# Kernel tuning notes

Measured on AMD Instinct MI355X. Metric: run time of the kernel, lower is better.

The kernel has to match this reference:

```python
import jax, jax.numpy as jnp
import numpy as np

EPS = 1e-8
PHI = (1 + 5 ** 0.5) / 2
B, S, D, H, L, O = 8, 2048, 256, 512, 3, 1
NH = 4
HD = H // NH


def setup_inputs() -> dict:
    key = jax.random.key(0)
    ks = jax.random.split(key, 12)
    g = lambda k, shape, s=0.02: jax.random.normal(k, shape, dtype=jnp.float32) * s
    # Fibonacci modular spiral embedding (fixed, requires_grad=False in torch)
    idx = jnp.arange(D, dtype=jnp.float32)
    r = (PHI * idx) % 1.0
    th = 2 * jnp.pi * r
    phase_emb = jnp.stack([r * jnp.cos(th), r * jnp.sin(th)], axis=1)  # [D,2]
    return dict(
        x=jax.random.normal(ks[0], (B, S, D), dtype=jnp.float32),
        proj_w=g(ks[1], (D, D), 0.06), proj_b=jnp.zeros((D,), jnp.float32),
        phase_emb=phase_emb,
        hebb_w=g(ks[2], (H, 2), 0.5),
        attn_in_w=g(ks[3], (L, 3 * H, H)), attn_in_b=jnp.zeros((L, 3 * H), jnp.float32),
        attn_out_w=g(ks[4], (L, H, H)), attn_out_b=jnp.zeros((L, H), jnp.float32),
        ff1_w=g(ks[5], (L, 4 * H, H)), ff1_b=jnp.zeros((L, 4 * H), jnp.float32),
        ff2_w=g(ks[6], (L, H, 4 * H)), ff2_b=jnp.zeros((L, H), jnp.float32),
        ln1_w=jnp.ones((L, H), jnp.float32), ln1_b=jnp.zeros((L, H), jnp.float32),
        ln2_w=jnp.ones((L, H), jnp.float32), ln2_b=jnp.zeros((L, H), jnp.float32),
        normA_w=jnp.ones((H,), jnp.float32), normA_b=jnp.zeros((H,), jnp.float32),
        normB_w=jnp.ones((H // 2,), jnp.float32), normB_b=jnp.zeros((H // 2,), jnp.float32),
        p1_w=g(ks[7], (H // 2, H), 0.04), p1_b=jnp.zeros((H // 2,), jnp.float32),
        p2_w=g(ks[8], (O, H // 2), 0.06), p2_b=jnp.zeros((O,), jnp.float32),
    )


def _ln(x, w, b, eps=1e-5):
    m = x.mean(-1, keepdims=True)
    v = ((x - m) ** 2).mean(-1, keepdims=True)
    return (x - m) * jax.lax.rsqrt(v + eps) * w + b


def _diffuse(psi, mask, dt, steps):
    # Norm-preserving RK2 integration of d(psi)/dt = mask@psi - psi
    def force(state):
        return jnp.einsum('bij,bjd->bid', mask, state) - state

    def step(p, _):
        r = jnp.linalg.norm(p, axis=-1, keepdims=True)
        k1 = force(p)
        ps = p + dt * k1
        ps = ps * (r / (jnp.linalg.norm(ps, axis=-1, keepdims=True) + EPS))
        k2 = force(ps)
        pn = p + 0.5 * dt * (k1 + k2)
        pn = pn * (r / (jnp.linalg.norm(pn, axis=-1, keepdims=True) + EPS))
        return pn, None

    psi, _ = jax.lax.scan(step, psi, None, length=steps)
    return psi


def _forward(x, proj_w, proj_b, phase_emb, hebb_w, attn_in_w, attn_in_b,
             attn_out_w, attn_out_b, ff1_w, ff1_b, ff2_w, ff2_b,
             ln1_w, ln1_b, ln2_w, ln2_b, normA_w, normA_b, normB_w, normB_b,
             p1_w, p1_b, p2_w, p2_b):
    b, s, _ = x.shape
    # PhaseHebbianEmbedder: project then map to 2D phase coords, unit-normalize
    xp = x @ proj_w.T + proj_b                               # [B,S,D]
    pc = jnp.einsum('bsd,dt->bst', xp, phase_emb)            # [B,S,2]
    psi = pc / (jnp.linalg.norm(pc, axis=-1, keepdims=True) + EPS)
    mask = jnp.broadcast_to(jnp.eye(s, dtype=x.dtype), (b, s, s))  # [B,S,S]
    psi = _diffuse(psi, mask, 0.1, 3)
    psi = _diffuse(psi, mask, 0.05, 4)
    A = jnp.einsum('bsd,btd->bst', psi, psi)                 # [B,S,S]
    final_psi = psi[:, -1]                                   # [B,2]
    h = (final_psi @ hebb_w.T)[:, None, :]                   # [B,1,H]
    for l in range(attn_in_w.shape[0]):
        qkv = h @ attn_in_w[l].T + attn_in_b[l]
        q, k, v = jnp.split(qkv, 3, axis=-1)
        hd = lambda t: t.reshape(b, -1, NH, HD).transpose(0, 2, 1, 3)
        q, k, v = hd(q), hd(k), hd(v)
        sc = jnp.einsum('bhqd,bhkd->bhqk', q, k) / jnp.sqrt(jnp.float32(HD))
        att = jax.nn.softmax(sc, axis=-1)
        o = jnp.einsum('bhqk,bhkd->bhqd', att, v).transpose(0, 2, 1, 3).reshape(b, -1, H)
        o = o @ attn_out_w[l].T + attn_out_b[l]
        h = _ln(h + o, ln1_w[l], ln1_b[l])
        ff = jax.nn.silu(h @ ff1_w[l].T + ff1_b[l]) @ ff2_w[l].T + ff2_b[l]
        h = _ln(h + ff, ln2_w[l], ln2_b[l])
    h = _ln(h[:, 0, :], normA_w, normA_b)
    p = jax.nn.silu(h @ p1_w.T + p1_b)
    p = _ln(p, normB_w, normB_b)
    preds = p @ p2_w.T + p2_b                                # [B,O]
    return preds, A, mask, psi


def reference(x, proj_w, proj_b, phase_emb, hebb_w, attn_in_w, attn_in_b,
              attn_out_w, attn_out_b, ff1_w, ff1_b, ff2_w, ff2_b,
              ln1_w, ln1_b, ln2_w, ln2_b, normA_w, normA_b, normB_w, normB_b,
              p1_w, p1_b, p2_w, p2_b):
    return _forward(x, proj_w, proj_b, phase_emb, hebb_w, attn_in_w, attn_in_b,
                    attn_out_w, attn_out_b, ff1_w, ff1_b, ff2_w, ff2_b,
                    ln1_w, ln1_b, ln2_w, ln2_b, normA_w, normA_b,
                    normB_w, normB_b, p1_w, p1_b, p2_w, p2_b)
```

## Files before the change

kernel.cpp:

```cpp
#include <hip/hip_runtime.h>
#include <hip/hip_bf16.h>

#define BB 8
#define SS 2048
#define DD 256
#define HH 512
#define LL 3
#define NROWS (BB * SS)

typedef float floatx4 __attribute__((ext_vector_type(4)));

__device__ __forceinline__ void amask_row(const float* __restrict__ psi,
                                          float* __restrict__ A, float* __restrict__ M,
                                          int blk)
{
    int tid = threadIdx.x;
    int b = blk >> 11, i = blk & (SS - 1);
    float2 pi = *reinterpret_cast<const float2*>(psi + (size_t)blk * 2);
    #pragma unroll
    for (int c = 0; c < 2; ++c) {
        int j0 = c * 1024 + tid * 4;
        const float4* pr = reinterpret_cast<const float4*>(psi + ((size_t)b * SS + j0) * 2);
        float4 q0 = pr[0], q1 = pr[1];
        floatx4 o;
        o.x = pi.x * q0.x + pi.y * q0.y;
        o.y = pi.x * q0.z + pi.y * q0.w;
        o.z = pi.x * q1.x + pi.y * q1.y;
        o.w = pi.x * q1.z + pi.y * q1.w;
        size_t rb = (size_t)blk * SS + j0;
        __builtin_nontemporal_store(o, reinterpret_cast<floatx4*>(A + rb));
        floatx4 m;
        m.x = (i == j0    ) ? 1.f : 0.f;
        m.y = (i == j0 + 1) ? 1.f : 0.f;
        m.z = (i == j0 + 2) ? 1.f : 0.f;
        m.w = (i == j0 + 3) ? 1.f : 0.f;
        __builtin_nontemporal_store(m, reinterpret_cast<floatx4*>(M + rb));
    }
}

__global__ void compute_M(const float* __restrict__ pw, const float* __restrict__ pb,
                          const float* __restrict__ pe, float* __restrict__ Mc)
{
    __shared__ float s0[4][256], s1[4][256];
    int tid = threadIdx.x;
    int k = tid & 255;
    int sub = tid >> 8;
    float a0 = 0.f, a1 = 0.f;
    #pragma unroll 8
    for (int d = sub * 64; d < sub * 64 + 64; ++d) {
        float w = pw[d * DD + k];
        a0 += w * pe[2 * d];
        a1 += w * pe[2 * d + 1];
    }
    s0[sub][k] = a0;
    s1[sub][k] = a1;
    __syncthreads();
    if (tid < 256) {
        Mc[2 * tid]     = s0[0][tid] + s0[1][tid] + s0[2][tid] + s0[3][tid];
        Mc[2 * tid + 1] = s1[0][tid] + s1[1][tid] + s1[2][tid] + s1[3][tid];
    }
    if (tid < 64) {
        float c0 = 0.f, c1 = 0.f;
        for (int d = tid; d < DD; d += 64) {
            c0 += pb[d] * pe[2 * d];
            c1 += pb[d] * pe[2 * d + 1];
        }
        #pragma unroll
        for (int dd = 32; dd; dd >>= 1) {
            c0 += __shfl_xor(c0, dd);
            c1 += __shfl_xor(c1, dd);
        }
        if (tid == 0) { Mc[512] = c0; Mc[513] = c1; }
    }
}

__global__ void psi_kernel(const float* __restrict__ x, const float* __restrict__ Mc,
                           float* __restrict__ psi)
{
    int tid = threadIdx.x;
    int wave = tid >> 6, lane = tid & 63;
    const float4* Mc4 = reinterpret_cast<const float4*>(Mc);
    float4 mA = Mc4[lane * 2];
    float4 mB = Mc4[lane * 2 + 1];
    float c0 = Mc[512], c1 = Mc[513];
    int base = blockIdx.x * 16 + wave * 4;
    #pragma unroll
    for (int it = 0; it < 4; ++it) {
        int rid = base + it;
        float4 v = *reinterpret_cast<const float4*>(x + (size_t)rid * DD + lane * 4);
        float a0 = v.x * mA.x + v.y * mA.z + v.z * mB.x + v.w * mB.z;
        float a1 = v.x * mA.y + v.y * mA.w + v.z * mB.y + v.w * mB.w;
        #pragma unroll
        for (int d = 32; d; d >>= 1) {
            a0 += __shfl_xor(a0, d);
            a1 += __shfl_xor(a1, d);
        }
        a0 += c0;
        a1 += c1;
        float n = sqrtf(a0 * a0 + a1 * a1);
        float scale = 1.f / (n + 1e-8f);
        float r = n * scale;
        #pragma unroll
        for (int i7 = 0; i7 < 7; ++i7) {
            float f = r / (r + 1e-8f);
            scale *= f;
            r *= f;
        }
        if (lane == 0) {
            float2 pv;
            pv.x = a0 * scale;
            pv.y = a1 * scale;
            *reinterpret_cast<float2*>(psi + (size_t)rid * 2) = pv;
        }
    }
}

__global__ void h0_kernel(const float* __restrict__ psi, const float* __restrict__ hebb,
                          float* __restrict__ h0,
                          float* __restrict__ Ao, float* __restrict__ Mo, int arow0)
{
    int bid = blockIdx.x;
    if (bid >= BB) {
        int r = arow0 + (bid - BB);
        if (r < NROWS) amask_row(psi, Ao, Mo, r);
        return;
    }
    float2 pv = *reinterpret_cast<const float2*>(psi + ((size_t)bid * SS + SS - 1) * 2);
    for (int j = threadIdx.x; j < HH; j += blockDim.x)
        h0[(size_t)bid * HH + j] = pv.x * hebb[2 * j] + pv.y * hebb[2 * j + 1];
}

__global__ void head_mm(const float* __restrict__ X, int K,
                        const float* __restrict__ xlnw, const float* __restrict__ xlnb,
                        const float* __restrict__ xln2w, const float* __restrict__ xln2b,
                        const float* __restrict__ W, const float* __restrict__ bias,
                        const float* __restrict__ res,
                        const float* __restrict__ reslnw, const float* __restrict__ reslnb,
                        float* __restrict__ out, int J, int G, int act,
                        const float* __restrict__ psi,
                        float* __restrict__ Ao, float* __restrict__ Mo,
                        int mmBlocks, int arow0)
{
    const int bid = blockIdx.x;
    if (bid >= mmBlocks) {
        int r = arow0 + (bid - mmBlocks);
        if (r < NROWS) amask_row(psi, Ao, Mo, r);
        return;
    }

    extern __shared__ float sX[];
    __shared__ float s_m[8], s_r[8], s_rm[8], s_rr[8];
    const int tid = threadIdx.x;
    const int row = tid >> 5, lane = tid & 31;
    const bool doLN = (xlnw != nullptr);
    const bool doRLN = (res != nullptr) && (reslnw != nullptr);

    if (doLN) {
        float s = 0.f, ss = 0.f;
        for (int k = lane; k < K; k += 32) {
            float v = X[row * K + k];
            s += v; ss += v * v;
        }
        for (int d = 16; d; d >>= 1) { s += __shfl_down(s, d); ss += __shfl_down(ss, d); }
        if (lane == 0) {
            float m = s / K;
            s_m[row] = m;
            s_r[row] = rsqrtf(ss / K - m * m + 1e-5f);
        }
    }
    if (doRLN) {
        float s = 0.f, ss = 0.f;
        for (int k = lane; k < J; k += 32) {
            float v = res[row * J + k];
            s += v; ss += v * v;
        }
        for (int d = 16; d; d >>= 1) { s += __shfl_down(s, d); ss += __shfl_down(ss, d); }
        if (lane == 0) {
            float m = s / J;
            s_rm[row] = m;
            s_rr[row] = rsqrtf(ss / J - m * m + 1e-5f);
        }
    }
    __syncthreads();

    if (doLN) {
        for (int idx = tid; idx < 8 * K; idx += 256) {
            int b = idx / K, k = idx - b * K;
            sX[idx] = (X[idx] - s_m[b]) * s_r[b] * xlnw[k] + xlnb[k];
        }
        __syncthreads();
        if (xln2w) {
            float s = 0.f, ss = 0.f;
            for (int k = lane; k < K; k += 32) {
                float v = sX[row * K + k];
                s += v; ss += v * v;
            }
            for (int d = 16; d; d >>= 1) { s += __shfl_down(s, d); ss += __shfl_down(ss, d); }
            if (lane == 0) {
                float m = s / K;
                s_m[row] = m;
                s_r[row] = rsqrtf(ss / K - m * m + 1e-5f);
            }
            __syncthreads();
            for (int idx = tid; idx < 8 * K; idx += 256) {
                int b = idx / K, k = idx - b * K;
                sX[idx] = (sX[idx] - s_m[b]) * s_r[b] * xln2w[k] + xln2b[k];
            }
            __syncthreads();
        }
    }

    const float* __restrict__ Xp = doLN ? (const float*)sX : X;
    const int g = tid & (G - 1);
    const int jj = tid / G;
    const int j = bid * (256 / G) + jj;

    float acc[8] = {0.f, 0.f, 0.f, 0.f, 0.f, 0.f, 0.f, 0.f};
    if (j < J) {
        const float4* W4 = reinterpret_cast<const float4*>(W + (size_t)j * K);
        const int K4 = K >> 2;
        for (int i4 = g; i4 < K4; i4 += G) {
            float4 w4 = W4[i4];
            int k = i4 << 2;
            #pragma unroll
            for (int b = 0; b < 8; ++b) {
                float4 xv = *reinterpret_cast<const float4*>(Xp + b * K + k);
                acc[b] = fmaf(w4.x, xv.x, acc[b]);
                acc[b] = fmaf(w4.y, xv.y, acc[b]);
                acc[b] = fmaf(w4.z, xv.z, acc[b]);
                acc[b] = fmaf(w4.w, xv.w, acc[b]);
            }
        }
    }
    for (int d = G >> 1; d; d >>= 1) {
        #pragma unroll
        for (int b = 0; b < 8; ++b) acc[b] += __shfl_down(acc[b], d);
    }
    if (g == 0 && j < J) {
        float bs = bias ? bias[j] : 0.f;
        #pragma unroll
        for (int b = 0; b < 8; ++b) {
            float v = acc[b] + bs;
            if (act) v = v / (1.f + expf(-v));
            if (res) {
                float rv = res[(size_t)b * J + j];
                if (reslnw) rv = (rv - s_rm[b]) * s_rr[b] * reslnw[j] + reslnb[j];
                v += rv;
            }
            out[(size_t)b * J + j] = v;
        }
    }
}

extern "C" void kernel_launch(void* const* d_in, const int* in_sizes, int n_in,
                              void* d_out, int out_size, void* d_ws, size_t ws_size,
                              hipStream_t stream)
{
    const float* x      = (const float*)d_in[0];
    const float* proj_w = (const float*)d_in[1];
    const float* proj_b = (const float*)d_in[2];
    const float* pe     = (const float*)d_in[3];
    const float* hebb   = (const float*)d_in[4];
    const float* ai_w   = (const float*)d_in[5];
    const float* ai_b   = (const float*)d_in[6];
    const float* ao_w   = (const float*)d_in[7];
    const float* ao_b   = (const float*)d_in[8];
    const float* f1_w   = (const float*)d_in[9];
    const float* f1_b   = (const float*)d_in[10];
    const float* f2_w   = (const float*)d_in[11];
    const float* f2_b   = (const float*)d_in[12];
    const float* ln1w   = (const float*)d_in[13];
    const float* ln1b   = (const float*)d_in[14];
    const float* ln2w   = (const float*)d_in[15];
    const float* ln2b   = (const float*)d_in[16];
    const float* nAw    = (const float*)d_in[17];
    const float* nAb    = (const float*)d_in[18];
    const float* nBw    = (const float*)d_in[19];
    const float* nBb    = (const float*)d_in[20];
    const float* p1w    = (const float*)d_in[21];
    const float* p1b    = (const float*)d_in[22];
    const float* p2w    = (const float*)d_in[23];
    const float* p2b    = (const float*)d_in[24];

    float* out   = (float*)d_out;
    float* preds = out;
    float* A     = out + 8;
    float* Mask  = out + 8 + (size_t)BB * SS * SS;
    float* Psi   = out + 8 + (size_t)2 * BB * SS * SS;

    float* ws = (float*)d_ws;
    float* Mc = ws;
    float* T  = ws + 640;
    float* V  = ws + 4736;
    float* T1 = ws + 8832;
    float* F  = ws + 12928;
    float* P  = ws + 29312;

    compute_M<<<1, 1024, 0, stream>>>(proj_w, proj_b, pe, Mc);
    psi_kernel<<<NROWS / 16, 256, 0, stream>>>(x, Mc, Psi);

    int ci = 0, arow = 0;
    auto nextq = [&]() { int q = 1092 + (ci < 4 ? 1 : 0); ++ci; return q; };

    {
        int q = nextq();
        h0_kernel<<<BB + q, 256, 0, stream>>>(Psi, hebb, T, A, Mask, arow);
        arow += q;
    }

    for (int l = 0; l < LL; ++l) {
        const float* pxw = l ? ln2w + (l - 1) * HH : nullptr;
        const float* pxb = l ? ln2b + (l - 1) * HH : nullptr;
        int q;
        q = nextq();
        head_mm<<<64 + q, 256, (pxw ? 8 * HH * 4 : 0), stream>>>(
            T, HH, pxw, pxb, nullptr, nullptr,
            ai_w + ((size_t)l * 3 * HH + 2 * HH) * HH, ai_b + l * 3 * HH + 2 * HH,
            nullptr, nullptr, nullptr, V, HH, 32, 0,
            Psi, A, Mask, 64, arow);
        arow += q;
        q = nextq();
        head_mm<<<64 + q, 256, 0, stream>>>(
            V, HH, nullptr, nullptr, nullptr, nullptr,
            ao_w + (size_t)l * HH * HH, ao_b + l * HH,
            T, pxw, pxb, T1, HH, 32, 0,
            Psi, A, Mask, 64, arow);
        arow += q;
        q = nextq();
        head_mm<<<128 + q, 256, 8 * HH * 4, stream>>>(
            T1, HH, ln1w + l * HH, ln1b + l * HH, nullptr, nullptr,
            f1_w + (size_t)l * 4 * HH * HH, f1_b + l * 4 * HH,
            nullptr, nullptr, nullptr, F, 4 * HH, 16, 1,
            Psi, A, Mask, 128, arow);
        arow += q;
        q = nextq();
        head_mm<<<128 + q, 256, 0, stream>>>(
            F, 4 * HH, nullptr, nullptr, nullptr, nullptr,
            f2_w + (size_t)l * HH * 4 * HH, f2_b + l * HH,
            T1, ln1w + l * HH, ln1b + l * HH, T, HH, 64, 0,
            Psi, A, Mask, 128, arow);
        arow += q;
    }
    {
        int q = nextq();
        head_mm<<<32 + q, 256, 8 * HH * 4, stream>>>(
            T, HH, ln2w + 2 * HH, ln2b + 2 * HH, nAw, nAb,
            p1w, p1b, nullptr, nullptr, nullptr, P, HH / 2, 32, 1,
            Psi, A, Mask, 32, arow);
        arow += q;
    }
    {
        int q = nextq();
        head_mm<<<1 + q, 256, 8 * (HH / 2) * 4, stream>>>(
            P, HH / 2, nBw, nBb, nullptr, nullptr,
            p2w, p2b, nullptr, nullptr, nullptr, preds, 1, 32, 0,
            Psi, A, Mask, 1, arow);
        arow += q;
    }
}
```

Baseline: 205.0 us.

## Fold value and output projections into one weight; fuse M, psi and h0 kernels

```diff
diff --git a/kernel.cpp b/kernel.cpp
--- a/kernel.cpp
+++ b/kernel.cpp
@@ -7,6 +7,8 @@
 #define HH 512
 #define LL 3
 #define NROWS (BB * SS)
+#define PSIBLK 1024
+#define WCBN 192
 
 typedef float floatx4 __attribute__((ext_vector_type(4)));
 
@@ -38,52 +40,87 @@
     }
 }
 
-__global__ void compute_M(const float* __restrict__ pw, const float* __restrict__ pb,
-                          const float* __restrict__ pe, float* __restrict__ Mc)
+__global__ void psiM_kernel(const float* __restrict__ x,
+                            const float* __restrict__ pw, const float* __restrict__ pb,
+                            const float* __restrict__ pe, const float* __restrict__ hebb,
+                            const float* __restrict__ ai_w, const float* __restrict__ ai_b,
+                            const float* __restrict__ ao_w, const float* __restrict__ ao_b,
+                            float* __restrict__ psi, float* __restrict__ h0,
+                            float* __restrict__ Wc, float* __restrict__ bc)
 {
-    __shared__ float s0[4][256], s1[4][256];
-    int tid = threadIdx.x;
-    int k = tid & 255;
-    int sub = tid >> 8;
-    float a0 = 0.f, a1 = 0.f;
-    #pragma unroll 8
-    for (int d = sub * 64; d < sub * 64 + 64; ++d) {
-        float w = pw[d * DD + k];
-        a0 += w * pe[2 * d];
-        a1 += w * pe[2 * d + 1];
-    }
-    s0[sub][k] = a0;
-    s1[sub][k] = a1;
+    __shared__ __align__(16) float sB[8 * HH];
+    const int tid = threadIdx.x;
+    const int bid = blockIdx.x;
+
+    if (bid >= PSIBLK) {
+        int wcb = bid - PSIBLK;
+        int l = wcb >> 6;
+        int j0 = (wcb & 63) * 8;
+        const float* WoB = ao_w + (size_t)l * HH * HH;
+        for (int idx = tid; idx < 8 * HH; idx += 256) {
+            int r = idx >> 9, m = idx & 511;
+            sB[idx] = WoB[(size_t)(j0 + r) * HH + m];
+        }
+        __syncthreads();
+        const float* WvB = ai_w + ((size_t)l * 3 * HH + 2 * HH) * HH;
+        int k0 = tid, k1 = tid + 256;
+        float acc0[8] = {0,0,0,0,0,0,0,0};
+        float acc1[8] = {0,0,0,0,0,0,0,0};
+        for (int m = 0; m < HH; ++m) {
+            float w0 = WvB[(size_t)m * HH + k0];
+            float w1 = WvB[(size_t)m * HH + k1];
+            #pragma unroll
+            for (int r = 0; r < 8; ++r) {
+                float wo = sB[r * HH + m];
+                acc0[r] = fmaf(wo, w0, acc0[r]);
+                acc1[r] = fmaf(wo, w1, acc1[r]);
+            }
+        }
+        #pragma unroll
+        for (int r = 0; r < 8; ++r) {
+            Wc[((size_t)l * HH + j0 + r) * HH + k0] = acc0[r];
+            Wc[((size_t)l * HH + j0 + r) * HH + k1] = acc1[r];
+        }
+        if (tid < 8) {
+            const float* bvB = ai_b + l * 3 * HH + 2 * HH;
+            float s = ao_b[l * HH + j0 + tid];
+            for (int m = 0; m < HH; ++m) s += sB[tid * HH + m] * bvB[m];
+            bc[l * HH + j0 + tid] = s;
+        }
+        return;
+    }
+
+    {
+        float a0 = 0.f, a1 = 0.f;
+        for (int d = 0; d < DD; ++d) {
+            float w = pw[d * DD + tid];
+            a0 += w * pe[2 * d];
+            a1 += w * pe[2 * d + 1];
+        }
+        sB[2 * tid] = a0;
+        sB[2 * tid + 1] = a1;
+        if (tid < 64) {
+            float c0 = 0.f, c1 = 0.f;
+            for (int d = tid; d < DD; d += 64) {
+                c0 += pb[d] * pe[2 * d];
+                c1 += pb[d] * pe[2 * d + 1];
+            }
+            #pragma unroll
+            for (int dd = 32; dd; dd >>= 1) {
+                c0 += __shfl_xor(c0, dd);
+                c1 += __shfl_xor(c1, dd);
+            }
+            if (tid == 0) { sB[512] = c0; sB[513] = c1; }
+        }
+    }
     __syncthreads();
-    if (tid < 256) {
-        Mc[2 * tid]     = s0[0][tid] + s0[1][tid] + s0[2][tid] + s0[3][tid];
-        Mc[2 * tid + 1] = s1[0][tid] + s1[1][tid] + s1[2][tid] + s1[3][tid];
-    }
-    if (tid < 64) {
-        float c0 = 0.f, c1 = 0.f;
-        for (int d = tid; d < DD; d += 64) {
-            c0 += pb[d] * pe[2 * d];
-            c1 += pb[d] * pe[2 * d + 1];
-        }
-        #pragma unroll
-        for (int dd = 32; dd; dd >>= 1) {
-            c0 += __shfl_xor(c0, dd);
-            c1 += __shfl_xor(c1, dd);
-        }
-        if (tid == 0) { Mc[512] = c0; Mc[513] = c1; }
-    }
-}
-
-__global__ void psi_kernel(const float* __restrict__ x, const float* __restrict__ Mc,
-                           float* __restrict__ psi)
-{
-    int tid = threadIdx.x;
+
     int wave = tid >> 6, lane = tid & 63;
-    const float4* Mc4 = reinterpret_cast<const float4*>(Mc);
-    float4 mA = Mc4[lane * 2];
-    float4 mB = Mc4[lane * 2 + 1];
-    float c0 = Mc[512], c1 = Mc[513];
-    int base = blockIdx.x * 16 + wave * 4;
+    const float4* sM4 = reinterpret_cast<const float4*>(sB);
+    float4 mA = sM4[lane * 2];
+    float4 mB = sM4[lane * 2 + 1];
+    float c0 = sB[512], c1 = sB[513];
+    int base = bid * 16 + wave * 4;
     #pragma unroll
     for (int it = 0; it < 4; ++it) {
         int rid = base + it;
@@ -106,28 +143,19 @@
             scale *= f;
             r *= f;
         }
+        float px = a0 * scale, py = a1 * scale;
         if (lane == 0) {
             float2 pv;
-            pv.x = a0 * scale;
-            pv.y = a1 * scale;
+            pv.x = px;
+            pv.y = py;
             *reinterpret_cast<float2*>(psi + (size_t)rid * 2) = pv;
         }
-    }
-}
-
-__global__ void h0_kernel(const float* __restrict__ psi, const float* __restrict__ hebb,
-                          float* __restrict__ h0,
-                          float* __restrict__ Ao, float* __restrict__ Mo, int arow0)
-{
-    int bid = blockIdx.x;
-    if (bid >= BB) {
-        int r = arow0 + (bid - BB);
-        if (r < NROWS) amask_row(psi, Ao, Mo, r);
-        return;
-    }
-    float2 pv = *reinterpret_cast<const float2*>(psi + ((size_t)bid * SS + SS - 1) * 2);
-    for (int j = threadIdx.x; j < HH; j += blockDim.x)
-        h0[(size_t)bid * HH + j] = pv.x * hebb[2 * j] + pv.y * hebb[2 * j + 1];
+        if ((rid & (SS - 1)) == SS - 1) {
+            int b = rid >> 11;
+            for (int j = lane; j < HH; j += 64)
+                h0[(size_t)b * HH + j] = px * hebb[2 * j] + py * hebb[2 * j + 1];
+        }
+    }
 }
 
 __global__ void head_mm(const float* __restrict__ X, int K,
@@ -288,25 +316,20 @@
     float* Mask  = out + 8 + (size_t)BB * SS * SS;
     float* Psi   = out + 8 + (size_t)2 * BB * SS * SS;
 
+    float* Wc = A + (size_t)15000 * SS;
+    float* bc = Wc + 3 * HH * HH;
+
     float* ws = (float*)d_ws;
-    float* Mc = ws;
     float* T  = ws + 640;
-    float* V  = ws + 4736;
     float* T1 = ws + 8832;
     float* F  = ws + 12928;
     float* P  = ws + 29312;
 
-    compute_M<<<1, 1024, 0, stream>>>(proj_w, proj_b, pe, Mc);
-    psi_kernel<<<NROWS / 16, 256, 0, stream>>>(x, Mc, Psi);
+    psiM_kernel<<<PSIBLK + WCBN, 256, 0, stream>>>(
+        x, proj_w, proj_b, pe, hebb, ai_w, ai_b, ao_w, ao_b, Psi, T, Wc, bc);
 
     int ci = 0, arow = 0;
-    auto nextq = [&]() { int q = 1092 + (ci < 4 ? 1 : 0); ++ci; return q; };
-
-    {
-        int q = nextq();
-        h0_kernel<<<BB + q, 256, 0, stream>>>(Psi, hebb, T, A, Mask, arow);
-        arow += q;
-    }
+    auto nextq = [&]() { int q = (ci < 10) ? 1490 : (NROWS - 1490 * 10); ++ci; return q; };
 
     for (int l = 0; l < LL; ++l) {
         const float* pxw = l ? ln2w + (l - 1) * HH : nullptr;
@@ -315,14 +338,7 @@
         q = nextq();
         head_mm<<<64 + q, 256, (pxw ? 8 * HH * 4 : 0), stream>>>(
             T, HH, pxw, pxb, nullptr, nullptr,
-            ai_w + ((size_t)l * 3 * HH + 2 * HH) * HH, ai_b + l * 3 * HH + 2 * HH,
-            nullptr, nullptr, nullptr, V, HH, 32, 0,
-            Psi, A, Mask, 64, arow);
-        arow += q;
-        q = nextq();
-        head_mm<<<64 + q, 256, 0, stream>>>(
-            V, HH, nullptr, nullptr, nullptr, nullptr,
-            ao_w + (size_t)l * HH * HH, ao_b + l * HH,
+            Wc + (size_t)l * HH * HH, bc + l * HH,
             T, pxw, pxb, T1, HH, 32, 0,
             Psi, A, Mask, 64, arow);
         arow += q;
```

After: 236.3 us. 15.3% more time.

## Fuse the whole head chain and the A/mask writes into one persistent mega kernel

Applied to the files above, without the earlier changes.

```diff
diff --git a/kernel.cpp b/kernel.cpp
--- a/kernel.cpp
+++ b/kernel.cpp
@@ -7,36 +7,10 @@
 #define HH 512
 #define LL 3
 #define NROWS (BB * SS)
+#define NWRK 8
+#define NSTB (NROWS / 4)
 
 typedef float floatx4 __attribute__((ext_vector_type(4)));
-
-__device__ __forceinline__ void amask_row(const float* __restrict__ psi,
-                                          float* __restrict__ A, float* __restrict__ M,
-                                          int blk)
-{
-    int tid = threadIdx.x;
-    int b = blk >> 11, i = blk & (SS - 1);
-    float2 pi = *reinterpret_cast<const float2*>(psi + (size_t)blk * 2);
-    #pragma unroll
-    for (int c = 0; c < 2; ++c) {
-        int j0 = c * 1024 + tid * 4;
-        const float4* pr = reinterpret_cast<const float4*>(psi + ((size_t)b * SS + j0) * 2);
-        float4 q0 = pr[0], q1 = pr[1];
-        floatx4 o;
-        o.x = pi.x * q0.x + pi.y * q0.y;
-        o.y = pi.x * q0.z + pi.y * q0.w;
-        o.z = pi.x * q1.x + pi.y * q1.y;
-        o.w = pi.x * q1.z + pi.y * q1.w;
-        size_t rb = (size_t)blk * SS + j0;
-        __builtin_nontemporal_store(o, reinterpret_cast<floatx4*>(A + rb));
-        floatx4 m;
-        m.x = (i == j0    ) ? 1.f : 0.f;
-        m.y = (i == j0 + 1) ? 1.f : 0.f;
-        m.z = (i == j0 + 2) ? 1.f : 0.f;
-        m.w = (i == j0 + 3) ? 1.f : 0.f;
-        __builtin_nontemporal_store(m, reinterpret_cast<floatx4*>(M + rb));
-    }
-}
 
 __global__ void compute_M(const float* __restrict__ pw, const float* __restrict__ pb,
                           const float* __restrict__ pe, float* __restrict__ Mc)
@@ -115,140 +89,152 @@
     }
 }
 
-__global__ void h0_kernel(const float* __restrict__ psi, const float* __restrict__ hebb,
-                          float* __restrict__ h0,
-                          float* __restrict__ Ao, float* __restrict__ Mo, int arow0)
-{
-    int bid = blockIdx.x;
-    if (bid >= BB) {
-        int r = arow0 + (bid - BB);
-        if (r < NROWS) amask_row(psi, Ao, Mo, r);
+__device__ __forceinline__ void ln_blk(const float* in, int N,
+                                       const float* __restrict__ w,
+                                       const float* __restrict__ bvec,
+                                       float* out, float* s_stat, int tid)
+{
+    if (tid < 64) {
+        float s = 0.f, ss = 0.f;
+        for (int k = tid; k < N; k += 64) {
+            float v = in[k];
+            s += v; ss += v * v;
+        }
+        #pragma unroll
+        for (int d = 32; d; d >>= 1) {
+            s += __shfl_xor(s, d);
+            ss += __shfl_xor(ss, d);
+        }
+        if (tid == 0) {
+            float m = s / N;
+            s_stat[0] = m;
+            s_stat[1] = rsqrtf(ss / N - m * m + 1e-5f);
+        }
+    }
+    __syncthreads();
+    float m = s_stat[0], r = s_stat[1];
+    for (int k = tid; k < N; k += 1024)
+        out[k] = (in[k] - m) * r * w[k] + bvec[k];
+    __syncthreads();
+}
+
+__device__ __forceinline__ void bgemm(const float* sXin, int K,
+                                      const float* __restrict__ W,
+                                      const float* __restrict__ bias,
+                                      const float* resLDS, float* outLDS,
+                                      int J, int G, int act, int tid)
+{
+    const int g = tid & (G - 1);
+    const int K4 = K >> 2;
+    const float4* X4 = reinterpret_cast<const float4*>(sXin);
+    for (int j = tid / G; j < J; j += 1024 / G) {
+        const float4* W4 = reinterpret_cast<const float4*>(W + (size_t)j * K);
+        float acc = 0.f;
+        for (int i4 = g; i4 < K4; i4 += G) {
+            float4 w = W4[i4];
+            float4 xv = X4[i4];
+            acc = fmaf(w.x, xv.x, acc);
+            acc = fmaf(w.y, xv.y, acc);
+            acc = fmaf(w.z, xv.z, acc);
+            acc = fmaf(w.w, xv.w, acc);
+        }
+        for (int d = G >> 1; d; d >>= 1) acc += __shfl_xor(acc, d);
+        if (g == 0) {
+            float v = acc + bias[j];
+            if (act) v = v / (1.f + expf(-v));
+            if (resLDS) v += resLDS[j];
+            outLDS[j] = v;
+        }
+    }
+    __syncthreads();
+}
+
+__global__ void __launch_bounds__(1024) mega(
+    const float* __restrict__ psi, const float* __restrict__ hebb,
+    const float* __restrict__ ai_w, const float* __restrict__ ai_b,
+    const float* __restrict__ ao_w, const float* __restrict__ ao_b,
+    const float* __restrict__ f1_w, const float* __restrict__ f1_b,
+    const float* __restrict__ f2_w, const float* __restrict__ f2_b,
+    const float* __restrict__ ln1w, const float* __restrict__ ln1b,
+    const float* __restrict__ ln2w, const float* __restrict__ ln2b,
+    const float* __restrict__ nAw, const float* __restrict__ nAb,
+    const float* __restrict__ nBw, const float* __restrict__ nBb,
+    const float* __restrict__ p1w, const float* __restrict__ p1b,
+    const float* __restrict__ p2w, const float* __restrict__ p2b,
+    float* __restrict__ preds, float* __restrict__ A, float* __restrict__ Mask)
+{
+    const int bid = blockIdx.x;
+    const int tid = threadIdx.x;
+
+    if (bid >= NWRK) {
+        int srow = tid >> 8, stid = tid & 255;
+        int blk = (bid - NWRK) * 4 + srow;
+        int b = blk >> 11, i = blk & (SS - 1);
+        float2 pi = *reinterpret_cast<const float2*>(psi + (size_t)blk * 2);
+        #pragma unroll
+        for (int c = 0; c < 2; ++c) {
+            int j0 = c * 1024 + stid * 4;
+            const float4* pr = reinterpret_cast<const float4*>(psi + ((size_t)b * SS + j0) * 2);
+            float4 q0 = pr[0], q1 = pr[1];
+            floatx4 o;
+            o.x = pi.x * q0.x + pi.y * q0.y;
+            o.y = pi.x * q0.z + pi.y * q0.w;
+            o.z = pi.x * q1.x + pi.y * q1.y;
+            o.w = pi.x * q1.z + pi.y * q1.w;
+            size_t rb = (size_t)blk * SS + j0;
+            __builtin_nontemporal_store(o, reinterpret_cast<floatx4*>(A + rb));
+            floatx4 m;
+            m.x = (i == j0    ) ? 1.f : 0.f;
+            m.y = (i == j0 + 1) ? 1.f : 0.f;
+            m.z = (i == j0 + 2) ? 1.f : 0.f;
+            m.w = (i == j0 + 3) ? 1.f : 0.f;
+            __builtin_nontemporal_store(m, reinterpret_cast<floatx4*>(Mask + rb));
+        }
         return;
     }
-    float2 pv = *reinterpret_cast<const float2*>(psi + ((size_t)bid * SS + SS - 1) * 2);
-    for (int j = threadIdx.x; j < HH; j += blockDim.x)
-        h0[(size_t)bid * HH + j] = pv.x * hebb[2 * j] + pv.y * hebb[2 * j + 1];
-}
-
-__global__ void head_mm(const float* __restrict__ X, int K,
-                        const float* __restrict__ xlnw, const float* __restrict__ xlnb,
-                        const float* __restrict__ xln2w, const float* __restrict__ xln2b,
-                        const float* __restrict__ W, const float* __restrict__ bias,
-                        const float* __restrict__ res,
-                        const float* __restrict__ reslnw, const float* __restrict__ reslnb,
-                        float* __restrict__ out, int J, int G, int act,
-                        const float* __restrict__ psi,
-                        float* __restrict__ Ao, float* __restrict__ Mo,
-                        int mmBlocks, int arow0)
-{
-    const int bid = blockIdx.x;
-    if (bid >= mmBlocks) {
-        int r = arow0 + (bid - mmBlocks);
-        if (r < NROWS) amask_row(psi, Ao, Mo, r);
-        return;
-    }
-
-    extern __shared__ float sX[];
-    __shared__ float s_m[8], s_r[8], s_rm[8], s_rr[8];
-    const int tid = threadIdx.x;
-    const int row = tid >> 5, lane = tid & 31;
-    const bool doLN = (xlnw != nullptr);
-    const bool doRLN = (res != nullptr) && (reslnw != nullptr);
-
-    if (doLN) {
-        float s = 0.f, ss = 0.f;
-        for (int k = lane; k < K; k += 32) {
-            float v = X[row * K + k];
-            s += v; ss += v * v;
-        }
-        for (int d = 16; d; d >>= 1) { s += __shfl_down(s, d); ss += __shfl_down(ss, d); }
-        if (lane == 0) {
-            float m = s / K;
-            s_m[row] = m;
-            s_r[row] = rsqrtf(ss / K - m * m + 1e-5f);
-        }
-    }
-    if (doRLN) {
-        float s = 0.f, ss = 0.f;
-        for (int k = lane; k < J; k += 32) {
-            float v = res[row * J + k];
-            s += v; ss += v * v;
-        }
-        for (int d = 16; d; d >>= 1) { s += __shfl_down(s, d); ss += __shfl_down(ss, d); }
-        if (lane == 0) {
-            float m = s / J;
-            s_rm[row] = m;
-            s_rr[row] = rsqrtf(ss / J - m * m + 1e-5f);
-        }
-    }
-    __syncthreads();
-
-    if (doLN) {
-        for (int idx = tid; idx < 8 * K; idx += 256) {
-            int b = idx / K, k = idx - b * K;
-            sX[idx] = (X[idx] - s_m[b]) * s_r[b] * xlnw[k] + xlnb[k];
-        }
-        __syncthreads();
-        if (xln2w) {
-            float s = 0.f, ss = 0.f;
-            for (int k = lane; k < K; k += 32) {
-                float v = sX[row * K + k];
-                s += v; ss += v * v;
-            }
-            for (int d = 16; d; d >>= 1) { s += __shfl_down(s, d); ss += __shfl_down(ss, d); }
-            if (lane == 0) {
-                float m = s / K;
-                s_m[row] = m;
-                s_r[row] = rsqrtf(ss / K - m * m + 1e-5f);
-            }
+
+    __shared__ __align__(16) float sT[HH];
+    __shared__ __align__(16) float sX0[HH];
+    __shared__ __align__(16) float sV[HH];
+    __shared__ __align__(16) float sF[4 * HH];
+    __shared__ __align__(16) float sP[HH / 2];
+    __shared__ float s_stat[2];
+    const int b = bid;
+
+    {
+        float2 pv = *reinterpret_cast<const float2*>(psi + ((size_t)b * SS + SS - 1) * 2);
+        for (int j = tid; j < HH; j += 1024)
+            sT[j] = pv.x * hebb[2 * j] + pv.y * hebb[2 * j + 1];
+    }
+    __syncthreads();
+
+    for (int l = 0; l < LL; ++l) {
+        if (l) {
+            ln_blk(sT, HH, ln2w + (l - 1) * HH, ln2b + (l - 1) * HH, sX0, s_stat, tid);
+        } else {
+            for (int k = tid; k < HH; k += 1024) sX0[k] = sT[k];
             __syncthreads();
-            for (int idx = tid; idx < 8 * K; idx += 256) {
-                int b = idx / K, k = idx - b * K;
-                sX[idx] = (sX[idx] - s_m[b]) * s_r[b] * xln2w[k] + xln2b[k];
-            }
-            __syncthreads();
-        }
-    }
-
-    const float* __restrict__ Xp = doLN ? (const float*)sX : X;
-    const int g = tid & (G - 1);
-    const int jj = tid / G;
-    const int j = bid * (256 / G) + jj;
-
-    float acc[8] = {0.f, 0.f, 0.f, 0.f, 0.f, 0.f, 0.f, 0.f};
-    if (j < J) {
-        const float4* W4 = reinterpret_cast<const float4*>(W + (size_t)j * K);
-        const int K4 = K >> 2;
-        for (int i4 = g; i4 < K4; i4 += G) {
-            float4 w4 = W4[i4];
-            int k = i4 << 2;
-            #pragma unroll
-            for (int b = 0; b < 8; ++b) {
-                float4 xv = *reinterpret_cast<const float4*>(Xp + b * K + k);
-                acc[b] = fmaf(w4.x, xv.x, acc[b]);
-                acc[b] = fmaf(w4.y, xv.y, acc[b]);
-                acc[b] = fmaf(w4.z, xv.z, acc[b]);
-                acc[b] = fmaf(w4.w, xv.w, acc[b]);
-            }
-        }
-    }
-    for (int d = G >> 1; d; d >>= 1) {
-        #pragma unroll
-        for (int b = 0; b < 8; ++b) acc[b] += __shfl_down(acc[b], d);
-    }
-    if (g == 0 && j < J) {
-        float bs = bias ? bias[j] : 0.f;
-        #pragma unroll
-        for (int b = 0; b < 8; ++b) {
-            float v = acc[b] + bs;
-            if (act) v = v / (1.f + expf(-v));
-            if (res) {
-                float rv = res[(size_t)b * J + j];
-                if (reslnw) rv = (rv - s_rm[b]) * s_rr[b] * reslnw[j] + reslnb[j];
-                v += rv;
-            }
-            out[(size_t)b * J + j] = v;
-        }
+        }
+        bgemm(sX0, HH, ai_w + ((size_t)l * 3 * HH + 2 * HH) * HH,
+              ai_b + l * 3 * HH + 2 * HH, nullptr, sV, HH, 2, 0, tid);
+        bgemm(sV, HH, ao_w + (size_t)l * HH * HH, ao_b + l * HH,
+              sX0, sT, HH, 2, 0, tid);
+        ln_blk(sT, HH, ln1w + l * HH, ln1b + l * HH, sX0, s_stat, tid);
+        bgemm(sX0, HH, f1_w + (size_t)l * 4 * HH * HH, f1_b + l * 4 * HH,
+              nullptr, sF, 4 * HH, 1, 1, tid);
+        bgemm(sF, 4 * HH, f2_w + (size_t)l * HH * 4 * HH, f2_b + l * HH,
+              sX0, sT, HH, 2, 0, tid);
+    }
+    ln_blk(sT, HH, ln2w + 2 * HH, ln2b + 2 * HH, sX0, s_stat, tid);
+    ln_blk(sX0, HH, nAw, nAb, sX0, s_stat, tid);
+    bgemm(sX0, HH, p1w, p1b, nullptr, sP, HH / 2, 4, 1, tid);
+    ln_blk(sP, HH / 2, nBw, nBb, sP, s_stat, tid);
+    if (tid < 64) {
+        float s = 0.f;
+        for (int k = tid; k < HH / 2; k += 64) s += sP[k] * p2w[k];
+        #pragma unroll
+        for (int d = 32; d; d >>= 1) s += __shfl_xor(s, d);
+        if (tid == 0) preds[b] = s + p2b[0];
     }
 }
 
@@ -290,71 +276,11 @@
 
     float* ws = (float*)d_ws;
     float* Mc = ws;
-    float* T  = ws + 640;
-    float* V  = ws + 4736;
-    float* T1 = ws + 8832;
-    float* F  = ws + 12928;
-    float* P  = ws + 29312;
 
     compute_M<<<1, 1024, 0, stream>>>(proj_w, proj_b, pe, Mc);
     psi_kernel<<<NROWS / 16, 256, 0, stream>>>(x, Mc, Psi);
-
-    int ci = 0, arow = 0;
-    auto nextq = [&]() { int q = 1092 + (ci < 4 ? 1 : 0); ++ci; return q; };
-
-    {
-        int q = nextq();
-        h0_kernel<<<BB + q, 256, 0, stream>>>(Psi, hebb, T, A, Mask, arow);
-        arow += q;
-    }
-
-    for (int l = 0; l < LL; ++l) {
-        const float* pxw = l ? ln2w + (l - 1) * HH : nullptr;
-        const float* pxb = l ? ln2b + (l - 1) * HH : nullptr;
-        int q;
-        q = nextq();
-        head_mm<<<64 + q, 256, (pxw ? 8 * HH * 4 : 0), stream>>>(
-            T, HH, pxw, pxb, nullptr, nullptr,
-            ai_w + ((size_t)l * 3 * HH + 2 * HH) * HH, ai_b + l * 3 * HH + 2 * HH,
-            nullptr, nullptr, nullptr, V, HH, 32, 0,
-            Psi, A, Mask, 64, arow);
-        arow += q;
-        q = nextq();
-        head_mm<<<64 + q, 256, 0, stream>>>(
-            V, HH, nullptr, nullptr, nullptr, nullptr,
-            ao_w + (size_t)l * HH * HH, ao_b + l * HH,
-            T, pxw, pxb, T1, HH, 32, 0,
-            Psi, A, Mask, 64, arow);
-        arow += q;
-        q = nextq();
-        head_mm<<<128 + q, 256, 8 * HH * 4, stream>>>(
-            T1, HH, ln1w + l * HH, ln1b + l * HH, nullptr, nullptr,
-            f1_w + (size_t)l * 4 * HH * HH, f1_b + l * 4 * HH,
-            nullptr, nullptr, nullptr, F, 4 * HH, 16, 1,
-            Psi, A, Mask, 128, arow);
-        arow += q;
-        q = nextq();
-        head_mm<<<128 + q, 256, 0, stream>>>(
-            F, 4 * HH, nullptr, nullptr, nullptr, nullptr,
-            f2_w + (size_t)l * HH * 4 * HH, f2_b + l * HH,
-            T1, ln1w + l * HH, ln1b + l * HH, T, HH, 64, 0,
-            Psi, A, Mask, 128, arow);
-        arow += q;
-    }
-    {
-        int q = nextq();
-        head_mm<<<32 + q, 256, 8 * HH * 4, stream>>>(
-            T, HH, ln2w + 2 * HH, ln2b + 2 * HH, nAw, nAb,
-            p1w, p1b, nullptr, nullptr, nullptr, P, HH / 2, 32, 1,
-            Psi, A, Mask, 32, arow);
-        arow += q;
-    }
-    {
-        int q = nextq();
-        head_mm<<<1 + q, 256, 8 * (HH / 2) * 4, stream>>>(
-            P, HH / 2, nBw, nBb, nullptr, nullptr,
-            p2w, p2b, nullptr, nullptr, nullptr, preds, 1, 32, 0,
-            Psi, A, Mask, 1, arow);
-        arow += q;
-    }
-}
+    mega<<<NWRK + NSTB, 1024, 0, stream>>>(
+        Psi, hebb, ai_w, ai_b, ao_w, ao_b, f1_w, f1_b, f2_w, f2_b,
+        ln1w, ln1b, ln2w, ln2b, nAw, nAb, nBw, nBb, p1w, p1b, p2w, p2b,
+        preds, A, Mask);
+}
```

New measurement: 814.8 us. +297.5%, slower.
